# Optimization experiments

Measured on AMD Instinct MI355X. Metric: run time of the kernel, lower is better.

The kernel has to match this reference:

```python
import jax, jax.numpy as jnp
import numpy as np

G = (1.0, 1.0)  # Clifford signature g = [1, 1]
MODES1 = 32
MODES2 = 32


def _clifford_kernel_2d(w, g):
    # w: (4, O, Cin, 2*m1, 2*m2); returns (4*O, 4*Cin, 2*m1, 2*m2)
    g0, g1 = g
    k0 = jnp.concatenate([w[0], g0 * w[1], g1 * w[2], -g0 * g1 * w[3]], axis=1)
    k1 = jnp.concatenate([w[1], w[0], -g1 * w[3], g1 * w[2]], axis=1)
    k2 = jnp.concatenate([w[2], g0 * w[3], w[0], -g0 * w[1]], axis=1)
    k3 = jnp.concatenate([w[3], w[2], -w[1], w[0]], axis=1)
    return jnp.concatenate([k0, k1, k2, k3], axis=0)


def _forward(x, weights):
    # x: (B, C, H, W, 4) multivector field
    B, C, H, W, I = x.shape
    m1, m2 = MODES1, MODES2
    # dual-pair complexification: (scalar, e12) and (e1, e2)
    d1 = jax.lax.complex(x[..., 0], x[..., 3])
    d2 = jax.lax.complex(x[..., 1], x[..., 2])
    d1f = jnp.fft.fft2(d1)  # over last two axes (H, W)
    d2f = jnp.fft.fft2(d2)
    # stacked blades in Fourier space: (B, 4*C, H, W)
    mv = jnp.concatenate([d1f.real, d2f.real, d2f.imag, d1f.imag], axis=1)
    # crop low-frequency corner modes into a (2*m1, 2*m2) block
    top = jnp.concatenate([mv[:, :, :m1, :m2], mv[:, :, :m1, -m2:]], axis=-1)
    bot = jnp.concatenate([mv[:, :, -m1:, :m2], mv[:, :, -m1:, -m2:]], axis=-1)
    inp = jnp.concatenate([top, bot], axis=-2)  # (B, 4*C, 2*m1, 2*m2)
    kernel = _clifford_kernel_2d(weights, G)  # (4*O, 4*C, 2*m1, 2*m2)
    out = jnp.einsum('bixy,oixy->boxy', inp, kernel)  # geometric-product mode mix
    O4 = kernel.shape[0]
    # scatter the four corners back into a zero-padded full spectrum
    out_ft = jnp.zeros((B, O4, H, W), dtype=x.dtype)
    out_ft = out_ft.at[:, :, :m1, :m2].set(out[:, :, :m1, :m2])
    out_ft = out_ft.at[:, :, -m1:, :m2].set(out[:, :, -m1:, :m2])
    out_ft = out_ft.at[:, :, :m1, -m2:].set(out[:, :, :m1, -m2:])
    out_ft = out_ft.at[:, :, -m1:, -m2:].set(out[:, :, -m1:, -m2:])
    # (B, 4, O, H, W) -> (B, O, H, W, 4)
    out_ft = out_ft.reshape(B, 4, O4 // 4, H, W).transpose(0, 2, 3, 4, 1)
    od1 = jax.lax.complex(out_ft[..., 0], out_ft[..., 3])
    od2 = jax.lax.complex(out_ft[..., 1], out_ft[..., 2])
    o1 = jnp.fft.ifft2(od1)
    o2 = jnp.fft.ifft2(od2)
    return jnp.stack([o1.real, o2.real, o2.imag, o1.imag], axis=-1)


def setup_inputs() -> dict:
    key = jax.random.key(0)
    kx, kw = jax.random.split(key)
    B, Cin, Cout, H, W = 4, 32, 32, 256, 256
    x = jax.random.normal(kx, (B, Cin, H, W, 4), dtype=jnp.float32)
    scale = 1.0 / (Cin * Cout)
    weights = scale * jax.random.uniform(kw, (4, Cout, Cin, 2 * MODES1, 2 * MODES2), dtype=jnp.float32)
    return {"x": x, "weights": weights}


def reference(x, weights):
    return _forward(x, weights)
```

## Files before the change

kernel.cpp:

```cpp
#include <hip/hip_runtime.h>
#include <math.h>

#define TWO_PI 6.28318530717958647692f

__device__ __forceinline__ void cmac(float2& a, const float2 b, const float2 c) {
  a.x = fmaf(b.x, c.x, fmaf(-b.y, c.y, a.x));
  a.y = fmaf(b.x, c.y, fmaf(b.y, c.x, a.y));
}

#define W16_C {1.f, 0.92387953f, 0.70710678f, 0.38268343f, 0.f, -0.38268343f, -0.70710678f, -0.92387953f, -1.f, -0.92387953f, -0.70710678f, -0.38268343f, 0.f, 0.38268343f, 0.70710678f, 0.92387953f}
#define W16_S {0.f, 0.38268343f, 0.70710678f, 0.92387953f, 1.f, 0.92387953f, 0.70710678f, 0.38268343f, 0.f, -0.38268343f, -0.70710678f, -0.92387953f, -1.f, -0.92387953f, -0.70710678f, -0.38268343f}

__device__ __forceinline__ void idft16_p1(const float2* a, const int p1,
                                          float2* X) {
  const float WC[16] = W16_C;
  const float WS[16] = W16_S;
  float2 tt[4];
#pragma unroll
  for (int r1 = 0; r1 < 4; ++r1) {
    const float2 q0 = a[r1], q1 = a[r1 + 4], q2 = a[r1 + 8], q3 = a[r1 + 12];
    const float2 s = make_float2(q0.x + q2.x, q0.y + q2.y);
    const float2 d = make_float2(q0.x - q2.x, q0.y - q2.y);
    const float2 u = make_float2(q1.x + q3.x, q1.y + q3.y);
    const float2 e = make_float2(q1.x - q3.x, q1.y - q3.y);
    float2 in;
    if (p1 == 0)      in = make_float2(s.x + u.x, s.y + u.y);
    else if (p1 == 1) in = make_float2(d.x - e.y, d.y + e.x);
    else if (p1 == 2) in = make_float2(s.x - u.x, s.y - u.y);
    else              in = make_float2(d.x + e.y, d.y - e.x);
    const float wc = WC[(r1 * p1) & 15], ws = WS[(r1 * p1) & 15];
    tt[r1] = make_float2(fmaf(in.x, wc, -in.y * ws), fmaf(in.y, wc, in.x * ws));
  }
  const float2 s = make_float2(tt[0].x + tt[2].x, tt[0].y + tt[2].y);
  const float2 d = make_float2(tt[0].x - tt[2].x, tt[0].y - tt[2].y);
  const float2 u = make_float2(tt[1].x + tt[3].x, tt[1].y + tt[3].y);
  const float2 e = make_float2(tt[1].x - tt[3].x, tt[1].y - tt[3].y);
  X[0] = make_float2(s.x + u.x, s.y + u.y);
  X[1] = make_float2(d.x - e.y, d.y + e.x);
  X[2] = make_float2(s.x - u.x, s.y - u.y);
  X[3] = make_float2(d.x + e.y, d.y - e.x);
}

__global__ __launch_bounds__(256) void f1_dft_h(const float* __restrict__ x,
                                                float* __restrict__ G) {
  __shared__ float2 twn[256];
  __shared__ float2 yf[64][4][2][8];
  const int t = threadIdx.x;
  {
    float sv, cv;
    sincosf(-TWO_PI * (float)t * (1.0f / 256.0f), &sv, &cv);
    twn[t] = make_float2(cv, sv);
  }
  const int bid = blockIdx.x;
  const int img = bid >> 5;
  const int w0  = (bid & 31) << 3;
  const float4* __restrict__ xb = (const float4*)x + (size_t)img * 65536 + w0;
  {
    const int wl  = t & 7;
    const int n1g = t >> 3;
#pragma unroll
    for (int ii = 0; ii < 2; ++ii) {
      const int n1 = n1g * 2 + ii;
      const float4 v0 = xb[(size_t)(n1)*256 + wl];
      const float4 v1 = xb[(size_t)(n1 + 64) * 256 + wl];
      const float4 v2 = xb[(size_t)(n1 + 128) * 256 + wl];
      const float4 v3 = xb[(size_t)(n1 + 192) * 256 + wl];
      {
        const float sx = v0.x + v2.x, sy = v0.w + v2.w;
        const float dx = v0.x - v2.x, dy = v0.w - v2.w;
        const float ux = v1.x + v3.x, uy = v1.w + v3.w;
        const float ex = v1.x - v3.x, ey = v1.w - v3.w;
        yf[n1][0][0][wl] = make_float2(sx + ux, sy + uy);
        yf[n1][2][0][wl] = make_float2(sx - ux, sy - uy);
        yf[n1][1][0][wl] = make_float2(dx + ey, dy - ex);
        yf[n1][3][0][wl] = make_float2(dx - ey, dy + ex);
      }
      {
        const float sx = v0.y + v2.y, sy = v0.z + v2.z;
        const float dx = v0.y - v2.y, dy = v0.z - v2.z;
        const float ux = v1.y + v3.y, uy = v1.z + v3.z;
        const float ex = v1.y - v3.y, ey = v1.z - v3.z;
        yf[n1][0][1][wl] = make_float2(sx + ux, sy + uy);
        yf[n1][2][1][wl] = make_float2(sx - ux, sy - uy);
        yf[n1][1][1][wl] = make_float2(dx + ey, dy - ex);
        yf[n1][3][1][wl] = make_float2(dx - ey, dy + ex);
      }
    }
  }
  __syncthreads();
  const int wl   = t & 7;
  const int dual = (t >> 3) & 1;
  const int kb   = t >> 4;
  const int r    = kb & 3;
  float2 acc[16];
#pragma unroll
  for (int c = 0; c < 16; ++c) acc[c] = make_float2(0.f, 0.f);
  int idx = 0;
#pragma unroll
  for (int n1 = 0; n1 < 64; ++n1) {
    const float2 tv = twn[idx];
    const float2 yv = yf[n1][r][dual][wl];
    cmac(acc[n1 & 15], yv, tv);
    idx = (idx + kb) & 255;
  }
  const float WC[16] = W16_C;
  const float WS[16] = W16_S;
  float2 D0 = make_float2(0.f, 0.f), D1 = D0, D2 = D0, D3 = D0;
#pragma unroll
  for (int c = 0; c < 16; ++c) {
    const float2 a = acc[c];
    const float cc = WC[c], ss = WS[c];
    const float cc2 = WC[(2 * c) & 15], ss2 = WS[(2 * c) & 15];
    D0.x += a.x;                         D0.y += a.y;
    D1.x = fmaf(a.x, cc,  fmaf( a.y, ss,  D1.x));
    D1.y = fmaf(a.y, cc,  fmaf(-a.x, ss,  D1.y));
    D2.x = fmaf(a.x, cc2, fmaf(-a.y, ss2, D2.x));
    D2.y = fmaf(a.y, cc2, fmaf( a.x, ss2, D2.y));
    D3.x = fmaf(a.x, cc,  fmaf(-a.y, ss,  D3.x));
    D3.y = fmaf(a.y, cc,  fmaf( a.x, ss,  D3.y));
  }
  float2* __restrict__ Gp = (float2*)G;
  const size_t base = ((size_t)(img * 2 + dual) * 64) * 256 + w0 + wl;
  Gp[base + (size_t)(kb)*256]      = D0;
  Gp[base + (size_t)(kb + 16)*256] = D1;
  Gp[base + (size_t)(kb + 32)*256] = D2;
  Gp[base + (size_t)(kb + 48)*256] = D3;
}

__global__ __launch_bounds__(256) void f2_dft_w(const float* __restrict__ G,
                                                float* __restrict__ mi) {
  __shared__ float2 twn[256];
  __shared__ float2 yf[16][65][4];
  const int t = threadIdx.x;
  {
    float sv, cv;
    sincosf(-TWO_PI * (float)t * (1.0f / 256.0f), &sv, &cv);
    twn[t] = make_float2(cv, sv);
  }
  const int row0 = blockIdx.x * 16;
  for (int idx = t; idx < 1024; idx += 256) {
    const int tr = idx >> 6, n1 = idx & 63;
    const float2* __restrict__ Gp = (const float2*)G + (size_t)(row0 + tr) * 256;
    const float2 z0 = Gp[n1], z1 = Gp[n1 + 64], z2 = Gp[n1 + 128], z3 = Gp[n1 + 192];
    const float sx = z0.x + z2.x, sy = z0.y + z2.y;
    const float dx = z0.x - z2.x, dy = z0.y - z2.y;
    const float ux = z1.x + z3.x, uy = z1.y + z3.y;
    const float ex = z1.x - z3.x, ey = z1.y - z3.y;
    yf[tr][n1][0] = make_float2(sx + ux, sy + uy);
    yf[tr][n1][2] = make_float2(sx - ux, sy - uy);
    yf[tr][n1][1] = make_float2(dx + ey, dy - ex);
    yf[tr][n1][3] = make_float2(dx - ey, dy + ex);
  }
  __syncthreads();
  const int kslot = t & 15;
  const int trow  = t >> 4;
  const int r     = kslot & 3;
  float2 acc[16];
#pragma unroll
  for (int c = 0; c < 16; ++c) acc[c] = make_float2(0.f, 0.f);
  int idx = 0;
#pragma unroll
  for (int n1 = 0; n1 < 64; ++n1) {
    const float2 tv = twn[idx];
    const float2 yv = yf[trow][n1][r];
    cmac(acc[n1 & 15], yv, tv);
    idx = (idx + kslot) & 255;
  }
  const float WC[16] = W16_C;
  const float WS[16] = W16_S;
  float2 D[4];
  D[0] = make_float2(0.f, 0.f); D[1] = D[0]; D[2] = D[0]; D[3] = D[0];
#pragma unroll
  for (int c = 0; c < 16; ++c) {
    const float2 a = acc[c];
    const float cc = WC[c], ss = WS[c];
    const float cc2 = WC[(2 * c) & 15], ss2 = WS[(2 * c) & 15];
    D[0].x += a.x;                        D[0].y += a.y;
    D[1].x = fmaf(a.x, cc,  fmaf( a.y, ss,  D[1].x));
    D[1].y = fmaf(a.y, cc,  fmaf(-a.x, ss,  D[1].y));
    D[2].x = fmaf(a.x, cc2, fmaf(-a.y, ss2, D[2].x));
    D[2].y = fmaf(a.y, cc2, fmaf( a.x, ss2, D[2].y));
    D[3].x = fmaf(a.x, cc,  fmaf(-a.y, ss,  D[3].x));
    D[3].y = fmaf(a.y, cc,  fmaf( a.x, ss,  D[3].y));
  }
  const int row  = row0 + trow;
  const int kx   = row & 63;
  const int dual = (row >> 6) & 1;
  const int bc   = row >> 7;
  const int b = bc >> 5, cc = bc & 31;
  const int sRe = dual ? 1 : 0;
  const int sIm = dual ? 2 : 3;
#pragma unroll
  for (int m = 0; m < 4; ++m) {
    const int kyi = kslot + (m << 4);
    const size_t moff = (size_t)kx * 64 + kyi;
    mi[(((size_t)(b * 4 + sRe)) * 32 + cc) * 4096 + moff] = D[m].x;
    mi[(((size_t)(b * 4 + sIm)) * 32 + cc) * 4096 + moff] = D[m].y;
  }
}

__global__ __launch_bounds__(256) void ein_k(const float* __restrict__ mi,
                                             const float* __restrict__ wgt,
                                             float* __restrict__ mo) {
  __shared__ float si[4][128][16];
  const int t = threadIdx.x;
  const int bid = blockIdx.x;
  const int m0 = (bid >> 1) << 4;
  const int oh = bid & 1;
  for (int idx = t; idx < 8192; idx += 256) {
    const int q = idx & 15, i = (idx >> 4) & 127, b = idx >> 11;
    si[b][i][q] = mi[((size_t)b * 128 + i) * 4096 + m0 + q];
  }
  __syncthreads();
  const int q = t & 15;
  const int o = oh * 16 + (t >> 4);
  const float* __restrict__ wb = wgt + (size_t)o * 32 * 4096 + m0 + q;
  float acc[4][4];
#pragma unroll
  for (int b = 0; b < 4; ++b)
#pragma unroll
    for (int r = 0; r < 4; ++r) acc[b][r] = 0.f;
  float wn[4];
#pragma unroll
  for (int j = 0; j < 4; ++j) wn[j] = wb[(size_t)j * 1024 * 4096];
#pragma unroll 1
  for (int c = 0; c < 32; ++c) {
    float wv[4];
#pragma unroll
    for (int j = 0; j < 4; ++j) wv[j] = wn[j];
    if (c < 31) {
#pragma unroll
      for (int j = 0; j < 4; ++j)
        wn[j] = wb[((size_t)j * 1024 + (c + 1)) * 4096];
    }
#pragma unroll
    for (int b = 0; b < 4; ++b) {
      const float iv0 = si[b][c][q];
      const float iv1 = si[b][32 + c][q];
      const float iv2 = si[b][64 + c][q];
      const float iv3 = si[b][96 + c][q];
      acc[b][0] += wv[0] * iv0 + wv[1] * iv1 + wv[2] * iv2 - wv[3] * iv3;
      acc[b][1] += wv[1] * iv0 + wv[0] * iv1 - wv[3] * iv2 + wv[2] * iv3;
      acc[b][2] += wv[2] * iv0 + wv[3] * iv1 + wv[0] * iv2 - wv[1] * iv3;
      acc[b][3] += wv[3] * iv0 + wv[2] * iv1 - wv[1] * iv2 + wv[0] * iv3;
    }
  }
#pragma unroll
  for (int b = 0; b < 4; ++b)
#pragma unroll
    for (int r = 0; r < 4; ++r)
      mo[(((size_t)b * 4 + r) * 32 + o) * 4096 + m0 + q] = acc[b][r];
}

__global__ __launch_bounds__(256) void i1_idft_w(const float* __restrict__ mo,
                                                 float* __restrict__ T) {
  __shared__ float2 twc[256];
  __shared__ float2 srow[16][66];
  const int t = threadIdx.x;
  {
    float sv, cv;
    sincosf(TWO_PI * (float)t * (1.0f / 256.0f), &sv, &cv);
    twc[t] = make_float2(cv, sv);
  }
  const int row0 = blockIdx.x * 16;
  for (int idx = t; idx < 1024; idx += 256) {
    const int tr = idx >> 6, ky = idx & 63;
    const int row = row0 + tr;
    const int kx = row & 63;
    const int dual = (row >> 6) & 1;
    const int bo = row >> 7;
    const int b = bo >> 5, o = bo & 31;
    const int rA = dual ? 1 : 0;
    const int rB = dual ? 2 : 3;
    const size_t ib = (size_t)kx * 64 + ky;
    srow[tr][ky] = make_float2(mo[(((size_t)b * 4 + rA) * 32 + o) * 4096 + ib],
                               mo[(((size_t)b * 4 + rB) * 32 + o) * 4096 + ib]);
  }
  __syncthreads();
  const int n1   = t & 15;
  const int trow = t >> 4;
  float2 a[16];
#pragma unroll
  for (int c = 0; c < 16; ++c) a[c] = make_float2(0.f, 0.f);
  int idx = 0;
#pragma unroll
  for (int kyi = 0; kyi < 64; ++kyi) {
    if (kyi == 32) idx = (idx + 192 * n1) & 255;
    cmac(a[kyi & 15], srow[trow][kyi], twc[idx]);
    idx = (idx + n1) & 255;
  }
  const int row = row0 + trow;
  float2* __restrict__ Tp = (float2*)T + (size_t)row * 256;
#pragma unroll
  for (int p1 = 0; p1 < 4; ++p1) {
    float2 X[4];
    idft16_p1(a, p1, X);
#pragma unroll
    for (int p2 = 0; p2 < 4; ++p2)
      Tp[n1 + 16 * (p1 + 4 * p2)] = X[p2];
  }
}

__global__ __launch_bounds__(256) void i2_idft_h(const float* __restrict__ T,
                                                 float* __restrict__ out) {
  __shared__ float2 twc[256];
  __shared__ float2 Tl[2][64][16];
  const int t = threadIdx.x;
  {
    float sv, cv;
    sincosf(TWO_PI * (float)t * (1.0f / 256.0f), &sv, &cv);
    twc[t] = make_float2(cv, sv);
  }
  const int bid = blockIdx.x;
  const int bo = bid >> 4;
  const int w0 = (bid & 15) << 4;
  const float2* __restrict__ Tp = (const float2*)T + (size_t)bo * 32768;
  for (int idx = t; idx < 2048; idx += 256) {
    const int ww = idx & 15, kxi = (idx >> 4) & 63, dual = idx >> 10;
    Tl[dual][kxi][ww] = Tp[((size_t)dual * 64 + kxi) * 256 + w0 + ww];
  }
  __syncthreads();
  const int wl = t & 15;
  const int n1 = t >> 4;
  float2 a0[16], a1[16];
#pragma unroll
  for (int c = 0; c < 16; ++c) {
    a0[c] = make_float2(0.f, 0.f);
    a1[c] = make_float2(0.f, 0.f);
  }
  int idx = 0;
#pragma unroll
  for (int kxi = 0; kxi < 64; ++kxi) {
    if (kxi == 32) idx = (idx + 192 * n1) & 255;
    const float2 tv = twc[idx];
    cmac(a0[kxi & 15], Tl[0][kxi][wl], tv);
    cmac(a1[kxi & 15], Tl[1][kxi][wl], tv);
    idx = (idx + n1) & 255;
  }
  const float sc = 1.0f / 65536.0f;
  float4* __restrict__ op = (float4*)out + (size_t)bo * 65536 + w0 + wl;
#pragma unroll
  for (int p1 = 0; p1 < 4; ++p1) {
    float2 X0[4], X1[4];
    idft16_p1(a0, p1, X0);
    idft16_p1(a1, p1, X1);
#pragma unroll
    for (int p2 = 0; p2 < 4; ++p2) {
      const int h = n1 + 16 * (p1 + 4 * p2);
      op[(size_t)h * 256] = make_float4(X0[p2].x * sc, X1[p2].x * sc,
                                        X1[p2].y * sc, X0[p2].y * sc);
    }
  }
}

extern "C" void kernel_launch(void* const* d_in, const int* in_sizes, int n_in,
                              void* d_out, int out_size, void* d_ws, size_t ws_size,
                              hipStream_t stream) {
  const float* x = (const float*)d_in[0];
  const float* wgt = (const float*)d_in[1];
  float* out = (float*)d_out;
  float* G  = (float*)d_ws;
  float* mi = G + 8388608;
  float* mo = mi + 2097152;

  hipLaunchKernelGGL(f1_dft_h, dim3(4096), dim3(256), 0, stream, x, G);
  hipLaunchKernelGGL(f2_dft_w, dim3(1024), dim3(256), 0, stream, G, mi);
  hipLaunchKernelGGL(ein_k,    dim3(512),  dim3(256), 0, stream, mi, wgt, mo);
  hipLaunchKernelGGL(i1_idft_w, dim3(1024), dim3(256), 0, stream, mo, G);
  hipLaunchKernelGGL(i2_idft_h, dim3(2048), dim3(256), 0, stream, G, out);
}
```

Baseline: 136.4 us.

## Store intermediate spectra as packed half2 and split einsum channel reduction

All intermediate workspace buffers (G, mi, mo, T) now hold packed fp16 complex pairs, which halves the global traffic between the five DFT and einsum stages. The first stage processes both dual channels per thread, staging its output through shared memory for coalesced stores. The einsum kernel runs with 512 threads, splits the channel reduction across two halves and combines them through shared memory. Using half precision for Fourier coefficients risks accuracy loss and possible overflow relative to the fp32 reference.

```diff
diff --git a/kernel.cpp b/kernel.cpp
--- a/kernel.cpp
+++ b/kernel.cpp
@@ -1,4 +1,5 @@
 #include <hip/hip_runtime.h>
+#include <hip/hip_fp16.h>
 #include <math.h>
 
 #define TWO_PI 6.28318530717958647692f
@@ -7,6 +8,10 @@
   a.x = fmaf(b.x, c.x, fmaf(-b.y, c.y, a.x));
   a.y = fmaf(b.x, c.y, fmaf(b.y, c.x, a.y));
 }
+__device__ __forceinline__ __half2 pkh(const float xx, const float yy) {
+  return __floats2half2_rn(xx, yy);
+}
+__device__ __forceinline__ float2 uph(const __half2 h) { return __half22float2(h); }
 
 #define W16_C {1.f, 0.92387953f, 0.70710678f, 0.38268343f, 0.f, -0.38268343f, -0.70710678f, -0.92387953f, -1.f, -0.92387953f, -0.70710678f, -0.38268343f, 0.f, 0.38268343f, 0.70710678f, 0.92387953f}
 #define W16_S {0.f, 0.38268343f, 0.70710678f, 0.92387953f, 1.f, 0.92387953f, 0.70710678f, 0.38268343f, 0.f, -0.38268343f, -0.70710678f, -0.92387953f, -1.f, -0.92387953f, -0.70710678f, -0.38268343f}
@@ -42,9 +47,10 @@
 }
 
 __global__ __launch_bounds__(256) void f1_dft_h(const float* __restrict__ x,
-                                                float* __restrict__ G) {
+                                                __half2* __restrict__ G) {
   __shared__ float2 twn[256];
-  __shared__ float2 yf[64][4][2][8];
+  __shared__ __half2 yf[64][4][20][2];
+  __shared__ __half2 dl[2][64][16];
   const int t = threadIdx.x;
   {
     float sv, cv;
@@ -52,15 +58,15 @@
     twn[t] = make_float2(cv, sv);
   }
   const int bid = blockIdx.x;
-  const int img = bid >> 5;
-  const int w0  = (bid & 31) << 3;
+  const int img = bid >> 4;
+  const int w0  = (bid & 15) << 4;
   const float4* __restrict__ xb = (const float4*)x + (size_t)img * 65536 + w0;
   {
-    const int wl  = t & 7;
-    const int n1g = t >> 3;
-#pragma unroll
-    for (int ii = 0; ii < 2; ++ii) {
-      const int n1 = n1g * 2 + ii;
+    const int wl  = t & 15;
+    const int n1g = t >> 4;
+#pragma unroll
+    for (int ii = 0; ii < 4; ++ii) {
+      const int n1 = n1g + (ii << 4);
       const float4 v0 = xb[(size_t)(n1)*256 + wl];
       const float4 v1 = xb[(size_t)(n1 + 64) * 256 + wl];
       const float4 v2 = xb[(size_t)(n1 + 128) * 256 + wl];
@@ -70,65 +76,94 @@
         const float dx = v0.x - v2.x, dy = v0.w - v2.w;
         const float ux = v1.x + v3.x, uy = v1.w + v3.w;
         const float ex = v1.x - v3.x, ey = v1.w - v3.w;
-        yf[n1][0][0][wl] = make_float2(sx + ux, sy + uy);
-        yf[n1][2][0][wl] = make_float2(sx - ux, sy - uy);
-        yf[n1][1][0][wl] = make_float2(dx + ey, dy - ex);
-        yf[n1][3][0][wl] = make_float2(dx - ey, dy + ex);
+        yf[n1][0][wl][0] = pkh(sx + ux, sy + uy);
+        yf[n1][2][wl][0] = pkh(sx - ux, sy - uy);
+        yf[n1][1][wl][0] = pkh(dx + ey, dy - ex);
+        yf[n1][3][wl][0] = pkh(dx - ey, dy + ex);
       }
       {
         const float sx = v0.y + v2.y, sy = v0.z + v2.z;
         const float dx = v0.y - v2.y, dy = v0.z - v2.z;
         const float ux = v1.y + v3.y, uy = v1.z + v3.z;
         const float ex = v1.y - v3.y, ey = v1.z - v3.z;
-        yf[n1][0][1][wl] = make_float2(sx + ux, sy + uy);
-        yf[n1][2][1][wl] = make_float2(sx - ux, sy - uy);
-        yf[n1][1][1][wl] = make_float2(dx + ey, dy - ex);
-        yf[n1][3][1][wl] = make_float2(dx - ey, dy + ex);
+        yf[n1][0][wl][1] = pkh(sx + ux, sy + uy);
+        yf[n1][2][wl][1] = pkh(sx - ux, sy - uy);
+        yf[n1][1][wl][1] = pkh(dx + ey, dy - ex);
+        yf[n1][3][wl][1] = pkh(dx - ey, dy + ex);
       }
     }
   }
   __syncthreads();
-  const int wl   = t & 7;
-  const int dual = (t >> 3) & 1;
-  const int kb   = t >> 4;
-  const int r    = kb & 3;
-  float2 acc[16];
-#pragma unroll
-  for (int c = 0; c < 16; ++c) acc[c] = make_float2(0.f, 0.f);
+  const int wl = t & 15;
+  const int kb = t >> 4;
+  const int r  = kb & 3;
+  float2 a0[16], a1[16];
+#pragma unroll
+  for (int c = 0; c < 16; ++c) {
+    a0[c] = make_float2(0.f, 0.f);
+    a1[c] = make_float2(0.f, 0.f);
+  }
   int idx = 0;
 #pragma unroll
   for (int n1 = 0; n1 < 64; ++n1) {
     const float2 tv = twn[idx];
-    const float2 yv = yf[n1][r][dual][wl];
-    cmac(acc[n1 & 15], yv, tv);
+    const float2 hv = *reinterpret_cast<const float2*>(&yf[n1][r][wl][0]);
+    const float2 y0 = uph(__builtin_bit_cast(__half2, hv.x));
+    const float2 y1 = uph(__builtin_bit_cast(__half2, hv.y));
+    cmac(a0[n1 & 15], y0, tv);
+    cmac(a1[n1 & 15], y1, tv);
     idx = (idx + kb) & 255;
   }
   const float WC[16] = W16_C;
   const float WS[16] = W16_S;
   float2 D0 = make_float2(0.f, 0.f), D1 = D0, D2 = D0, D3 = D0;
+  float2 E0 = D0, E1 = D0, E2 = D0, E3 = D0;
 #pragma unroll
   for (int c = 0; c < 16; ++c) {
-    const float2 a = acc[c];
     const float cc = WC[c], ss = WS[c];
     const float cc2 = WC[(2 * c) & 15], ss2 = WS[(2 * c) & 15];
-    D0.x += a.x;                         D0.y += a.y;
-    D1.x = fmaf(a.x, cc,  fmaf( a.y, ss,  D1.x));
-    D1.y = fmaf(a.y, cc,  fmaf(-a.x, ss,  D1.y));
-    D2.x = fmaf(a.x, cc2, fmaf(-a.y, ss2, D2.x));
-    D2.y = fmaf(a.y, cc2, fmaf( a.x, ss2, D2.y));
-    D3.x = fmaf(a.x, cc,  fmaf(-a.y, ss,  D3.x));
-    D3.y = fmaf(a.y, cc,  fmaf( a.x, ss,  D3.y));
-  }
-  float2* __restrict__ Gp = (float2*)G;
-  const size_t base = ((size_t)(img * 2 + dual) * 64) * 256 + w0 + wl;
-  Gp[base + (size_t)(kb)*256]      = D0;
-  Gp[base + (size_t)(kb + 16)*256] = D1;
-  Gp[base + (size_t)(kb + 32)*256] = D2;
-  Gp[base + (size_t)(kb + 48)*256] = D3;
-}
-
-__global__ __launch_bounds__(256) void f2_dft_w(const float* __restrict__ G,
-                                                float* __restrict__ mi) {
+    {
+      const float2 a = a0[c];
+      D0.x += a.x;                         D0.y += a.y;
+      D1.x = fmaf(a.x, cc,  fmaf( a.y, ss,  D1.x));
+      D1.y = fmaf(a.y, cc,  fmaf(-a.x, ss,  D1.y));
+      D2.x = fmaf(a.x, cc2, fmaf(-a.y, ss2, D2.x));
+      D2.y = fmaf(a.y, cc2, fmaf( a.x, ss2, D2.y));
+      D3.x = fmaf(a.x, cc,  fmaf(-a.y, ss,  D3.x));
+      D3.y = fmaf(a.y, cc,  fmaf( a.x, ss,  D3.y));
+    }
+    {
+      const float2 a = a1[c];
+      E0.x += a.x;                         E0.y += a.y;
+      E1.x = fmaf(a.x, cc,  fmaf( a.y, ss,  E1.x));
+      E1.y = fmaf(a.y, cc,  fmaf(-a.x, ss,  E1.y));
+      E2.x = fmaf(a.x, cc2, fmaf(-a.y, ss2, E2.x));
+      E2.y = fmaf(a.y, cc2, fmaf( a.x, ss2, E2.y));
+      E3.x = fmaf(a.x, cc,  fmaf(-a.y, ss,  E3.x));
+      E3.y = fmaf(a.y, cc,  fmaf( a.x, ss,  E3.y));
+    }
+  }
+  dl[0][kb][wl]      = pkh(D0.x, D0.y);
+  dl[0][kb + 16][wl] = pkh(D1.x, D1.y);
+  dl[0][kb + 32][wl] = pkh(D2.x, D2.y);
+  dl[0][kb + 48][wl] = pkh(D3.x, D3.y);
+  dl[1][kb][wl]      = pkh(E0.x, E0.y);
+  dl[1][kb + 16][wl] = pkh(E1.x, E1.y);
+  dl[1][kb + 32][wl] = pkh(E2.x, E2.y);
+  dl[1][kb + 48][wl] = pkh(E3.x, E3.y);
+  __syncthreads();
+  const __half2* __restrict__ dfl = &dl[0][0][0];
+#pragma unroll
+  for (int i = 0; i < 8; ++i) {
+    const int flat = t + (i << 8);
+    const int dual = flat >> 10, kx = (flat >> 4) & 63, w = flat & 15;
+    const size_t row = (size_t)(img * 2 + dual) * 64 + kx;
+    G[row * 256 + w0 + w] = dfl[flat];
+  }
+}
+
+__global__ __launch_bounds__(256) void f2_dft_w(const __half2* __restrict__ G,
+                                                __half2* __restrict__ mi) {
   __shared__ float2 twn[256];
   __shared__ float2 yf[16][65][4];
   const int t = threadIdx.x;
@@ -140,8 +175,9 @@
   const int row0 = blockIdx.x * 16;
   for (int idx = t; idx < 1024; idx += 256) {
     const int tr = idx >> 6, n1 = idx & 63;
-    const float2* __restrict__ Gp = (const float2*)G + (size_t)(row0 + tr) * 256;
-    const float2 z0 = Gp[n1], z1 = Gp[n1 + 64], z2 = Gp[n1 + 128], z3 = Gp[n1 + 192];
+    const __half2* __restrict__ Gp = G + (size_t)(row0 + tr) * 256;
+    const float2 z0 = uph(Gp[n1]), z1 = uph(Gp[n1 + 64]);
+    const float2 z2 = uph(Gp[n1 + 128]), z3 = uph(Gp[n1 + 192]);
     const float sx = z0.x + z2.x, sy = z0.y + z2.y;
     const float dx = z0.x - z2.x, dy = z0.y - z2.y;
     const float ux = z1.x + z3.x, uy = z1.y + z3.y;
@@ -188,50 +224,53 @@
   const int dual = (row >> 6) & 1;
   const int bc   = row >> 7;
   const int b = bc >> 5, cc = bc & 31;
-  const int sRe = dual ? 1 : 0;
-  const int sIm = dual ? 2 : 3;
 #pragma unroll
   for (int m = 0; m < 4; ++m) {
     const int kyi = kslot + (m << 4);
-    const size_t moff = (size_t)kx * 64 + kyi;
-    mi[(((size_t)(b * 4 + sRe)) * 32 + cc) * 4096 + moff] = D[m].x;
-    mi[(((size_t)(b * 4 + sIm)) * 32 + cc) * 4096 + moff] = D[m].y;
-  }
-}
-
-__global__ __launch_bounds__(256) void ein_k(const float* __restrict__ mi,
+    mi[((size_t)((b * 2 + dual) * 32 + cc)) * 4096 + kx * 64 + kyi] =
+        pkh(D[m].x, D[m].y);
+  }
+}
+
+__global__ __launch_bounds__(512) void ein_k(const __half2* __restrict__ mi,
                                              const float* __restrict__ wgt,
-                                             float* __restrict__ mo) {
+                                             __half2* __restrict__ mo) {
   __shared__ float si[4][128][16];
   const int t = threadIdx.x;
   const int bid = blockIdx.x;
   const int m0 = (bid >> 1) << 4;
   const int oh = bid & 1;
-  for (int idx = t; idx < 8192; idx += 256) {
-    const int q = idx & 15, i = (idx >> 4) & 127, b = idx >> 11;
-    si[b][i][q] = mi[((size_t)b * 128 + i) * 4096 + m0 + q];
-  }
-  __syncthreads();
-  const int q = t & 15;
-  const int o = oh * 16 + (t >> 4);
-  const float* __restrict__ wb = wgt + (size_t)o * 32 * 4096 + m0 + q;
+  for (int idx = t; idx < 4096; idx += 512) {
+    const int q = idx & 15, c = (idx >> 4) & 31, dual = (idx >> 9) & 1, b = idx >> 10;
+    const float2 f = uph(mi[((size_t)((b * 2 + dual) * 32 + c)) * 4096 + m0 + q]);
+    if (dual == 0) { si[b][c][q] = f.x;      si[b][96 + c][q] = f.y; }
+    else           { si[b][32 + c][q] = f.x; si[b][64 + c][q] = f.y; }
+  }
+  __syncthreads();
+  const int q  = t & 15;
+  const int o  = oh * 16 + ((t >> 4) & 15);
+  const int ch = t >> 8;
+  const int c0 = ch << 4;
+  const float* __restrict__ wb = wgt + (size_t)o * 131072 + m0 + q;
   float acc[4][4];
 #pragma unroll
   for (int b = 0; b < 4; ++b)
 #pragma unroll
     for (int r = 0; r < 4; ++r) acc[b][r] = 0.f;
-  float wn[4];
-#pragma unroll
-  for (int j = 0; j < 4; ++j) wn[j] = wb[(size_t)j * 1024 * 4096];
+  float wA[4], wB[4];
+#pragma unroll
+  for (int j = 0; j < 4; ++j) wA[j] = wb[(size_t)j * 4194304 + (size_t)c0 * 4096];
+#pragma unroll
+  for (int j = 0; j < 4; ++j) wB[j] = wb[(size_t)j * 4194304 + (size_t)(c0 + 1) * 4096];
 #pragma unroll 1
-  for (int c = 0; c < 32; ++c) {
+  for (int c = c0; c < c0 + 16; ++c) {
     float wv[4];
 #pragma unroll
-    for (int j = 0; j < 4; ++j) wv[j] = wn[j];
-    if (c < 31) {
+    for (int j = 0; j < 4; ++j) { wv[j] = wA[j]; wA[j] = wB[j]; }
+    if (c + 2 < c0 + 16) {
 #pragma unroll
       for (int j = 0; j < 4; ++j)
-        wn[j] = wb[((size_t)j * 1024 + (c + 1)) * 4096];
+        wB[j] = wb[(size_t)j * 4194304 + (size_t)(c + 2) * 4096];
     }
 #pragma unroll
     for (int b = 0; b < 4; ++b) {
@@ -245,15 +284,31 @@
       acc[b][3] += wv[3] * iv0 + wv[2] * iv1 - wv[1] * iv2 + wv[0] * iv3;
     }
   }
-#pragma unroll
-  for (int b = 0; b < 4; ++b)
-#pragma unroll
-    for (int r = 0; r < 4; ++r)
-      mo[(((size_t)b * 4 + r) * 32 + o) * 4096 + m0 + q] = acc[b][r];
-}
-
-__global__ __launch_bounds__(256) void i1_idft_w(const float* __restrict__ mo,
-                                                 float* __restrict__ T) {
+  __syncthreads();
+  float* __restrict__ red = &si[0][0][0];
+  if (ch == 1) {
+    const int tt = t & 255;
+#pragma unroll
+    for (int b = 0; b < 4; ++b)
+#pragma unroll
+      for (int r = 0; r < 4; ++r) red[tt * 17 + b * 4 + r] = acc[b][r];
+  }
+  __syncthreads();
+  if (ch == 0) {
+#pragma unroll
+    for (int b = 0; b < 4; ++b)
+#pragma unroll
+      for (int r = 0; r < 4; ++r) acc[b][r] += red[t * 17 + b * 4 + r];
+#pragma unroll
+    for (int b = 0; b < 4; ++b) {
+      mo[((size_t)((b * 2 + 0) * 32 + o)) * 4096 + m0 + q] = pkh(acc[b][0], acc[b][3]);
+      mo[((size_t)((b * 2 + 1) * 32 + o)) * 4096 + m0 + q] = pkh(acc[b][1], acc[b][2]);
+    }
+  }
+}
+
+__global__ __launch_bounds__(256) void i1_idft_w(const __half2* __restrict__ mo,
+                                                 __half2* __restrict__ T) {
   __shared__ float2 twc[256];
   __shared__ float2 srow[16][66];
   const int t = threadIdx.x;
@@ -270,11 +325,8 @@
     const int dual = (row >> 6) & 1;
     const int bo = row >> 7;
     const int b = bo >> 5, o = bo & 31;
-    const int rA = dual ? 1 : 0;
-    const int rB = dual ? 2 : 3;
-    const size_t ib = (size_t)kx * 64 + ky;
-    srow[tr][ky] = make_float2(mo[(((size_t)b * 4 + rA) * 32 + o) * 4096 + ib],
-                               mo[(((size_t)b * 4 + rB) * 32 + o) * 4096 + ib]);
+    srow[tr][ky] =
+        uph(mo[((size_t)((b * 2 + dual) * 32 + o)) * 4096 + kx * 64 + ky]);
   }
   __syncthreads();
   const int n1   = t & 15;
@@ -290,18 +342,18 @@
     idx = (idx + n1) & 255;
   }
   const int row = row0 + trow;
-  float2* __restrict__ Tp = (float2*)T + (size_t)row * 256;
+  __half2* __restrict__ Tp = T + (size_t)row * 256;
 #pragma unroll
   for (int p1 = 0; p1 < 4; ++p1) {
     float2 X[4];
     idft16_p1(a, p1, X);
 #pragma unroll
     for (int p2 = 0; p2 < 4; ++p2)
-      Tp[n1 + 16 * (p1 + 4 * p2)] = X[p2];
-  }
-}
-
-__global__ __launch_bounds__(256) void i2_idft_h(const float* __restrict__ T,
+      Tp[n1 + 16 * (p1 + 4 * p2)] = pkh(X[p2].x, X[p2].y);
+  }
+}
+
+__global__ __launch_bounds__(256) void i2_idft_h(const __half2* __restrict__ T,
                                                  float* __restrict__ out) {
   __shared__ float2 twc[256];
   __shared__ float2 Tl[2][64][16];
@@ -314,10 +366,10 @@
   const int bid = blockIdx.x;
   const int bo = bid >> 4;
   const int w0 = (bid & 15) << 4;
-  const float2* __restrict__ Tp = (const float2*)T + (size_t)bo * 32768;
+  const __half2* __restrict__ Tp = T + (size_t)bo * 32768;
   for (int idx = t; idx < 2048; idx += 256) {
     const int ww = idx & 15, kxi = (idx >> 4) & 63, dual = idx >> 10;
-    Tl[dual][kxi][ww] = Tp[((size_t)dual * 64 + kxi) * 256 + w0 + ww];
+    Tl[dual][kxi][ww] = uph(Tp[((size_t)dual * 64 + kxi) * 256 + w0 + ww]);
   }
   __syncthreads();
   const int wl = t & 15;
@@ -359,13 +411,13 @@
   const float* x = (const float*)d_in[0];
   const float* wgt = (const float*)d_in[1];
   float* out = (float*)d_out;
-  float* G  = (float*)d_ws;
-  float* mi = G + 8388608;
-  float* mo = mi + 2097152;
-
-  hipLaunchKernelGGL(f1_dft_h, dim3(4096), dim3(256), 0, stream, x, G);
+  __half2* G  = (__half2*)d_ws;
+  __half2* mi = G + 4194304;
+  __half2* mo = mi + 1048576;
+
+  hipLaunchKernelGGL(f1_dft_h, dim3(2048), dim3(256), 0, stream, x, G);
   hipLaunchKernelGGL(f2_dft_w, dim3(1024), dim3(256), 0, stream, G, mi);
-  hipLaunchKernelGGL(ein_k,    dim3(512),  dim3(256), 0, stream, mi, wgt, mo);
+  hipLaunchKernelGGL(ein_k,    dim3(512),  dim3(512), 0, stream, mi, wgt, mo);
   hipLaunchKernelGGL(i1_idft_w, dim3(1024), dim3(256), 0, stream, mo, G);
   hipLaunchKernelGGL(i2_idft_h, dim3(2048), dim3(256), 0, stream, G, out);
 }
```

Result: faster. 126.3 us, median of 2 (-7.4%).
